# Kernel tuning notes

Hardware: AMD Instinct MI355X
Metric: run time of the kernel (lower is better)

Reference implementation:

```python
import jax, jax.numpy as jnp
import numpy as np

NT, NS, NH, NG = 365, 1024, 64, 32
NW = NH * 8 + 2


def setup_inputs() -> dict:
    key = jax.random.key(0)
    k1, k2, k3, k4 = jax.random.split(key, 4)
    std = 1.0 / np.sqrt(NH)
    x = jax.random.normal(k1, (NT, NS, 4), dtype=jnp.float32)
    # make P (precip) nonnegative and T1 < T2 plausible-ish; math is still generic
    xc = jax.random.normal(k2, (NS, NG), dtype=jnp.float32)
    fc_w = jax.random.uniform(k3, (NW, NG), minval=-std, maxval=std, dtype=jnp.float32)
    fc_b = jax.random.uniform(k4, (NW,), minval=-std, maxval=std, dtype=jnp.float32)
    return {"x": x, "xc": xc, "fc_w": fc_w, "fc_b": fc_b}


def reference(x, xc, fc_w, fc_b):
    nh = NH
    P, E, T1, T2 = x[..., 0], x[..., 1], x[..., 2], x[..., 3]  # each [nt, ns]
    Ta = (T1 + T2) * 0.5
    # rain/snow partition: rP = 1 - arccos((T1+T2)/(T2-T1))/3.1415, masked
    valid = (T1 < 0) & (T2 > 0)
    denom = jnp.where(valid, T2 - T1, 1.0)
    ratio = jnp.clip(jnp.where(valid, (T1 + T2) / denom, 0.0), -0.999999, 0.999999)
    rP = 1.0 - jnp.arccos(ratio) / 3.1415
    rP = jnp.where(T1 >= 0, 1.0, rP)
    rP = jnp.where(T2 <= 0, 0.0, rP)
    Ps = (1.0 - rP) * P  # snow   [nt, ns]
    Pl = rP * P          # liquid [nt, ns]

    w = xc @ fc_w.T + fc_b  # [ns, nh*8+2]
    gm = jnp.exp(w[:, :nh]) + 1.0
    ge = jax.nn.sigmoid(w[:, nh:2 * nh]) * 2.0
    go = jax.nn.sigmoid(w[:, 2 * nh:3 * nh])
    gl = jnp.exp(w[:, 3 * nh:4 * nh] * 2.0)
    ga = jax.nn.softmax(w[:, 4 * nh:5 * nh], axis=1)  # Dropout in eval mode = identity
    gb = jax.nn.sigmoid(w[:, 5 * nh:6 * nh])
    qb = jax.nn.relu(w[:, -1]) / nh  # [ns]
    kb = jax.nn.sigmoid(w[:, 6 * nh:7 * nh]) / 10.0
    gi = jax.nn.sigmoid(w[:, 7 * nh:8 * nh])

    ns = P.shape[1]
    init = (jnp.zeros((ns, nh), jnp.float32),) * 3  # S0, H0, G0

    def step(carry, inp):
        S0, H0, G0 = carry
        Ps_k, Pl_k, Ta_k, E_k = inp  # each [ns]
        S = S0 + Ps_k[:, None]
        Sm = jnp.minimum(S0, jax.nn.relu(Ta_k[:, None] * gm))  # snowmelt
        H = jax.nn.relu(H0 + Sm + Pl_k[:, None] * gi - E_k[:, None] * ge)
        Q1 = jax.nn.relu(H - gl)
        Q2a = jnp.minimum(H, gl) * go
        Q2 = Q2a * (1.0 - gb)
        G = G0 + Q2a * gb
        Q3 = G * kb
        H0n = jnp.minimum(H - Q2a, gl)
        G0n = G - Q3
        S0n = S - Sm
        Y = jnp.sum((Q1 + Q2 + Q3 + qb[:, None]) * ga, axis=1)  # [ns]
        return (S0n, H0n, G0n), Y

    _, Yout = jax.lax.scan(step, init, (Ps, Pl, Ta, E))
    return Yout  # [nt, ns]
```

## Files before the change

kernel.cpp:

```cpp
#include <hip/hip_runtime.h>
#include <math.h>

#define NT_ 365
#define NS_ 1024
#define NH_ 64
#define NG_ 32
#define NW_ 514
#define CH_ 64
#define NCHUNK_ 6
#define YPAD_ 65

__device__ __forceinline__ float sigmoidf(float v) {
  return 1.0f / (1.0f + expf(-v));
}

__device__ __forceinline__ float4 compute_met(float4 xv) {
  const float P = xv.x, E = xv.y, T1 = xv.z, T2 = xv.w;
  const float Ta = (T1 + T2) * 0.5f;
  float rP;
  if (T2 <= 0.0f) {
    rP = 0.0f;
  } else if (T1 >= 0.0f) {
    rP = 1.0f;
  } else {
    float r = (T1 + T2) / (T2 - T1);
    r = fminf(fmaxf(r, -0.999999f), 0.999999f);
    rP = 1.0f - acosf(r) * (1.0f / 3.1415f);
  }
  float4 m;
  m.x = (1.0f - rP) * P;
  m.y = rP * P;
  m.z = fmaxf(Ta, 0.0f);
  m.w = E;
  return m;
}

__global__ __launch_bounds__(256) void waternet_scan(
    const float* __restrict__ x,
    const float* __restrict__ xc,
    const float* __restrict__ fc_w,
    const float* __restrict__ fc_b,
    float* __restrict__ out)
{
  __shared__ float  ytile[4][2][CH_ * YPAD_];
  __shared__ float4 smet[4][CH_];

  const int tid  = threadIdx.x;
  const int lane = tid & 63;
  const int wv   = tid >> 6;
  const int site = (blockIdx.x << 2) + wv;
  const int us   = __builtin_amdgcn_readfirstlane(site);
  const float4* xp = (const float4*)x;

  float4 xcur = xp[lane * NS_ + site];

  float acc[8];
#pragma unroll
  for (int k = 0; k < 8; ++k) acc[k] = fc_b[k * NH_ + lane];
  float accq = fc_b[NW_ - 1];

  const float4* xcq = (const float4*)(xc + us * NG_);
  const float4* wq4 = (const float4*)fc_w;
#pragma unroll
  for (int g4 = 0; g4 < NG_ / 4; ++g4) {
    const float4 xv = xcq[g4];
#pragma unroll
    for (int k = 0; k < 8; ++k) {
      const float4 w = wq4[(k * NH_ + lane) * (NG_ / 4) + g4];
      acc[k] = fmaf(xv.x, w.x, acc[k]);
      acc[k] = fmaf(xv.y, w.y, acc[k]);
      acc[k] = fmaf(xv.z, w.z, acc[k]);
      acc[k] = fmaf(xv.w, w.w, acc[k]);
    }
    {
      const float4 w = wq4[(NW_ - 1) * (NG_ / 4) + g4];
      accq = fmaf(xv.x, w.x, accq);
      accq = fmaf(xv.y, w.y, accq);
      accq = fmaf(xv.z, w.z, accq);
      accq = fmaf(xv.w, w.w, accq);
    }
  }

  const float gm = expf(acc[0]) + 1.0f;
  const float ge = sigmoidf(acc[1]) * 2.0f;
  const float go = sigmoidf(acc[2]);
  const float gl = expf(acc[3] * 2.0f);
  float mx = acc[4];
#pragma unroll
  for (int mm = 32; mm >= 1; mm >>= 1) mx = fmaxf(mx, __shfl_xor(mx, mm, 64));
  const float ex = expf(acc[4] - mx);
  float sm = ex;
#pragma unroll
  for (int mm = 32; mm >= 1; mm >>= 1) sm += __shfl_xor(sm, mm, 64);
  const float ga = ex / sm;
  const float gb = sigmoidf(acc[5]);
  const float kb = sigmoidf(acc[6]) * 0.1f;
  const float gi = sigmoidf(acc[7]);
  const float qb = fmaxf(accq, 0.0f) * (1.0f / NH_);
  const float kb1m = 1.0f - kb;
  const float nge  = -ge;
  const float gq1  = go * (1.0f - gb) - 1.0f;

  float S0 = 0.0f, H0 = 0.0f, G0 = 0.0f;
  const int vofs = lane * NS_ + site;

  smet[wv][lane] = compute_met(xcur);

  auto step = [&](const float4 mt, float* ywaddr) {
    const float melt = mt.z * gm;
    const float dmx  = fmaxf(S0 - melt, 0.0f);
    const float hs   = H0 + S0;
    S0 = dmx + mt.x;
    const float t3 = fmaf(mt.y, gi, hs - dmx);
    const float H  = fmaxf(fmaf(mt.w, nge, t3), 0.0f);
    const float M  = fminf(H, gl);
    const float Q2a = M * go;
    H0 = fminf(H - Q2a, gl);
    const float G = fmaf(Q2a, gb, G0);
    G0 = G * kb1m;
    *ywaddr = fmaf(G, kb, fmaf(M, gq1, H)) * ga;
  };

  {
    float4 xnext = xp[(CH_ + lane) * NS_ + site];
    float* yw = &ytile[wv][0][lane];
    const float4* mp = &smet[wv][0];
#pragma unroll
    for (int j = 0; j < CH_; ++j) step(mp[j], yw + j * YPAD_);
    smet[wv][lane] = compute_met(xnext);
  }

  for (int c = 1; c < NCHUNK_; ++c) {
    int tn = (c + 1) * CH_ + lane;
    tn = (tn < NT_) ? tn : (NT_ - 1);
    const float4 xnext = xp[tn * NS_ + site];

    float*       yw = &ytile[wv][c & 1][lane];
    const float* yr = &ytile[wv][(c - 1) & 1][lane * YPAD_];
    const float4* mp = &smet[wv][0];
    float r0 = 0.0f, r1 = 0.0f, r2 = 0.0f, r3 = 0.0f;
#pragma unroll
    for (int j = 0; j < CH_; ++j) {
      if ((j & 3) == 0) {
        r0 += yr[j + 0];
        r1 += yr[j + 1];
        r2 += yr[j + 2];
        r3 += yr[j + 3];
      }
      step(mp[j], yw + j * YPAD_);
    }
    out[vofs + (c - 1) * CH_ * NS_] = ((r0 + r1) + (r2 + r3)) + qb;
    smet[wv][lane] = compute_met(xnext);
  }

  {
    const float* yr = &ytile[wv][1][lane * YPAD_];
    float r0 = 0.0f, r1 = 0.0f, r2 = 0.0f, r3 = 0.0f;
#pragma unroll
    for (int h = 0; h < CH_; h += 4) {
      r0 += yr[h + 0];
      r1 += yr[h + 1];
      r2 += yr[h + 2];
      r3 += yr[h + 3];
    }
    if (lane < NT_ - 5 * CH_)
      out[vofs + 5 * CH_ * NS_] = ((r0 + r1) + (r2 + r3)) + qb;
  }
}

extern "C" void kernel_launch(void* const* d_in, const int* in_sizes, int n_in,
                              void* d_out, int out_size, void* d_ws, size_t ws_size,
                              hipStream_t stream) {
  const float* x    = (const float*)d_in[0];
  const float* xc   = (const float*)d_in[1];
  const float* fc_w = (const float*)d_in[2];
  const float* fc_b = (const float*)d_in[3];
  float* out = (float*)d_out;

  hipLaunchKernelGGL(waternet_scan, dim3(NS_ / 4), dim3(256), 0, stream,
                     x, xc, fc_w, fc_b, out);
}
```

Before: 90.21 us.

## Single-buffer the y tile and pack eight sites per block

Drops the double-buffered ytile: each chunk now writes its 64 steps, then immediately reduces the tile and stores the output, instead of overlapping the previous chunk's reduction with the current chunk's scan. Blocks grow from 4 to 8 waves (128 blocks of 512 threads). This halves LDS per wave and simplifies the loop, but it serialises the reduction after the scan and leaves only 128 blocks to cover the device.

Measured after the change: 98.21 us. +8.9%, slower.

```diff
diff --git a/kernel.cpp b/kernel.cpp
--- a/kernel.cpp
+++ b/kernel.cpp
@@ -9,6 +9,7 @@
 #define CH_ 64
 #define NCHUNK_ 6
 #define YPAD_ 65
+#define WPB_ 8
 
 __device__ __forceinline__ float sigmoidf(float v) {
   return 1.0f / (1.0f + expf(-v));
@@ -35,20 +36,20 @@
   return m;
 }
 
-__global__ __launch_bounds__(256) void waternet_scan(
+__global__ __launch_bounds__(512) void waternet_scan(
     const float* __restrict__ x,
     const float* __restrict__ xc,
     const float* __restrict__ fc_w,
     const float* __restrict__ fc_b,
     float* __restrict__ out)
 {
-  __shared__ float  ytile[4][2][CH_ * YPAD_];
-  __shared__ float4 smet[4][CH_];
+  __shared__ float  ytile[WPB_][CH_ * YPAD_];
+  __shared__ float4 smet[WPB_][CH_];
 
   const int tid  = threadIdx.x;
   const int lane = tid & 63;
   const int wv   = tid >> 6;
-  const int site = (blockIdx.x << 2) + wv;
+  const int site = (blockIdx.x << 3) + wv;
   const int us   = __builtin_amdgcn_readfirstlane(site);
   const float4* xp = (const float4*)x;
 
@@ -102,7 +103,6 @@
   const float gq1  = go * (1.0f - gb) - 1.0f;
 
   float S0 = 0.0f, H0 = 0.0f, G0 = 0.0f;
-  const int vofs = lane * NS_ + site;
 
   smet[wv][lane] = compute_met(xcur);
 
@@ -121,40 +121,18 @@
     *ywaddr = fmaf(G, kb, fmaf(M, gq1, H)) * ga;
   };
 
-  {
-    float4 xnext = xp[(CH_ + lane) * NS_ + site];
-    float* yw = &ytile[wv][0][lane];
-    const float4* mp = &smet[wv][0];
-#pragma unroll
-    for (int j = 0; j < CH_; ++j) step(mp[j], yw + j * YPAD_);
-    smet[wv][lane] = compute_met(xnext);
-  }
+  float*       yw = &ytile[wv][lane];
+  const float* yr = &ytile[wv][lane * YPAD_];
 
-  for (int c = 1; c < NCHUNK_; ++c) {
+  for (int c = 0; c < NCHUNK_; ++c) {
     int tn = (c + 1) * CH_ + lane;
     tn = (tn < NT_) ? tn : (NT_ - 1);
     const float4 xnext = xp[tn * NS_ + site];
 
-    float*       yw = &ytile[wv][c & 1][lane];
-    const float* yr = &ytile[wv][(c - 1) & 1][lane * YPAD_];
     const float4* mp = &smet[wv][0];
-    float r0 = 0.0f, r1 = 0.0f, r2 = 0.0f, r3 = 0.0f;
 #pragma unroll
-    for (int j = 0; j < CH_; ++j) {
-      if ((j & 3) == 0) {
-        r0 += yr[j + 0];
-        r1 += yr[j + 1];
-        r2 += yr[j + 2];
-        r3 += yr[j + 3];
-      }
-      step(mp[j], yw + j * YPAD_);
-    }
-    out[vofs + (c - 1) * CH_ * NS_] = ((r0 + r1) + (r2 + r3)) + qb;
-    smet[wv][lane] = compute_met(xnext);
-  }
+    for (int j = 0; j < CH_; ++j) step(mp[j], yw + j * YPAD_);
 
-  {
-    const float* yr = &ytile[wv][1][lane * YPAD_];
     float r0 = 0.0f, r1 = 0.0f, r2 = 0.0f, r3 = 0.0f;
 #pragma unroll
     for (int h = 0; h < CH_; h += 4) {
@@ -163,8 +141,10 @@
       r2 += yr[h + 2];
       r3 += yr[h + 3];
     }
-    if (lane < NT_ - 5 * CH_)
-      out[vofs + 5 * CH_ * NS_] = ((r0 + r1) + (r2 + r3)) + qb;
+    const int t_out = c * CH_ + lane;
+    if (t_out < NT_) out[t_out * NS_ + site] = ((r0 + r1) + (r2 + r3)) + qb;
+
+    if (c + 1 < NCHUNK_) smet[wv][lane] = compute_met(xnext);
   }
 }
 
@@ -177,6 +157,6 @@
   const float* fc_b = (const float*)d_in[3];
   float* out = (float*)d_out;
 
-  hipLaunchKernelGGL(waternet_scan, dim3(NS_ / 4), dim3(256), 0, stream,
+  hipLaunchKernelGGL(waternet_scan, dim3(NS_ / WPB_), dim3(WPB_ * 64), 0, stream,
                      x, xc, fc_w, fc_b, out);
 }
```
